# Kernel optimization log

Hardware: AMD Instinct MI355X
Metric: run time of the kernel (lower is better)

## Reference

```python
import jax, jax.numpy as jnp
import numpy as np

D, H, DK, L, F, V = 512, 16, 32, 16, 1024, 32768
C1, C2, CORE, LG, MD, B = 512, 256, 256, 64, 64, 16
T_IN = C1 + C2 + CORE      # 1024
T_TF = CORE + LG + MD      # 384


def _ln(x, g, b, eps=1e-5):
    mu = x.mean(-1, keepdims=True)
    var = ((x - mu) ** 2).mean(-1, keepdims=True)
    return (x - mu) * jax.lax.rsqrt(var + eps) * g + b


def _heads(x):  # [B,T,D] -> [B,H,T,DK]
    b, t, _ = x.shape
    return x.reshape(b, t, H, DK).transpose(0, 2, 1, 3)


def _summarizer(ids, sem, pos, inw, inb, outw, outb, tok, lng, lnb):
    b, t = ids.shape
    x = sem[ids] + pos[:t][None]                      # [B,T,D]
    wq, wk, wv = jnp.split(inw, 3, axis=0)
    bq, bk, bv = jnp.split(inb, 3, axis=0)
    q = _heads(jnp.broadcast_to(tok, (b, tok.shape[1], D)) @ wq.T + bq)
    k = _heads(x @ wk.T + bk)
    v = _heads(x @ wv.T + bv)
    s = jnp.einsum('bhqd,bhkd->bhqk', q, k) / jnp.sqrt(jnp.float32(DK))
    a = jax.nn.softmax(s, axis=-1)
    o = jnp.einsum('bhqk,bhkd->bhqd', a, v).transpose(0, 2, 1, 3).reshape(b, -1, D)
    return _ln(o @ outw.T + outb, lng, lnb)


def _forward(emb_sem, emb_pos,
             lg_sem, lg_pos, lg_inw, lg_inb, lg_outw, lg_outb, lg_tok, lg_lng, lg_lnb,
             md_sem, md_pos, md_inw, md_inb, md_outw, md_outb, md_tok, md_lng, md_lnb,
             qkv_w, qkv_b, wo_w, wo_b, ln1_g, ln1_b, ln2_g, ln2_b,
             ff1_w, ff1_b, ff2_w, ff2_b, hd_lng, hd_lnb, hd_w, hd_b,
             input_ids, target_ids):
    lg_ids = input_ids[:, -(C1 + C2 + CORE):-(C2 + CORE)]
    md_ids = input_ids[:, -(C2 + CORE):-CORE]
    core_ids = input_ids[:, -CORE:]
    tgt = target_ids[:, -CORE:]

    lg_emb = _summarizer(lg_ids, lg_sem, lg_pos, lg_inw, lg_inb, lg_outw, lg_outb, lg_tok, lg_lng, lg_lnb)
    md_emb = _summarizer(md_ids, md_sem, md_pos, md_inw, md_inb, md_outw, md_outb, md_tok, md_lng, md_lnb)
    x_core = emb_sem[core_ids] + emb_pos[:CORE][None]
    x = jnp.concatenate([lg_emb, md_emb, x_core], axis=1)   # [B, 384, D]

    mask = jnp.tril(jnp.ones((T_TF, T_TF), dtype=bool))

    def step(x, p):
        qw, qb, ow, ob, g1, b1, g2, b2, f1w, f1b, f2w, f2b = p
        h = _ln(x, g1, b1)
        qkv = h @ qw.T + qb
        q, k, v = (_heads(t) for t in jnp.split(qkv, 3, axis=-1))
        s = jnp.einsum('bhqd,bhkd->bhqk', q, k) / jnp.sqrt(jnp.float32(DK))
        s = jnp.where(mask, s, -jnp.inf)
        a = jax.nn.softmax(s, axis=-1)
        o = jnp.einsum('bhqk,bhkd->bhqd', a, v).transpose(0, 2, 1, 3).reshape(x.shape)
        x = x + o @ ow.T + ob
        h2 = _ln(x, g2, b2)
        ff = jax.nn.gelu(h2 @ f1w.T + f1b, approximate=False) @ f2w.T + f2b
        return x + ff, None

    x, _ = jax.lax.scan(step, x, (qkv_w, qkv_b, wo_w, wo_b, ln1_g, ln1_b,
                                  ln2_g, ln2_b, ff1_w, ff1_b, ff2_w, ff2_b))
    logits = (_ln(x, hd_lng, hd_lnb) @ hd_w.T + hd_b)[:, -CORE:, :]
    return logits, tgt


def setup_inputs() -> dict:
    key = jax.random.key(0)
    ks = jax.random.split(key, 24)
    def rn(k, shape, s=0.02):
        return jax.random.normal(k, shape, jnp.float32) * s
    z, o = jnp.zeros, jnp.ones
    return {
        'input_ids': jax.random.randint(ks[0], (B, T_IN), 0, V),
        'target_ids': jax.random.randint(ks[1], (B, T_IN), 0, V),
        'emb_sem': rn(ks[2], (V, D)), 'emb_pos': rn(ks[3], (CORE, D)),
        'lg_sem': rn(ks[4], (V, D)), 'lg_pos': rn(ks[5], (C1, D)),
        'lg_inw': rn(ks[6], (3 * D, D)), 'lg_inb': z(3 * D),
        'lg_outw': rn(ks[7], (D, D)), 'lg_outb': z(D),
        'lg_tok': rn(ks[8], (1, LG, D), 1.0), 'lg_lng': o(D), 'lg_lnb': z(D),
        'md_sem': rn(ks[9], (V, D)), 'md_pos': rn(ks[10], (C2, D)),
        'md_inw': rn(ks[11], (3 * D, D)), 'md_inb': z(3 * D),
        'md_outw': rn(ks[12], (D, D)), 'md_outb': z(D),
        'md_tok': rn(ks[13], (1, MD, D), 1.0), 'md_lng': o(D), 'md_lnb': z(D),
        'qkv_w': rn(ks[14], (L, 3 * D, D)), 'qkv_b': z((L, 3 * D)),
        'wo_w': rn(ks[15], (L, D, D)), 'wo_b': z((L, D)),
        'ln1_g': o((L, D)), 'ln1_b': z((L, D)), 'ln2_g': o((L, D)), 'ln2_b': z((L, D)),
        'ff1_w': rn(ks[16], (L, F, D)), 'ff1_b': z((L, F)),
        'ff2_w': rn(ks[17], (L, D, F)), 'ff2_b': z((L, D)),
        'hd_lng': o(D), 'hd_lnb': z(D), 'hd_w': rn(ks[18], (V, D)), 'hd_b': z(V),
    }


def reference(input_ids, target_ids, emb_sem, emb_pos,
              lg_sem, lg_pos, lg_inw, lg_inb, lg_outw, lg_outb, lg_tok, lg_lng, lg_lnb,
              md_sem, md_pos, md_inw, md_inb, md_outw, md_outb, md_tok, md_lng, md_lnb,
              qkv_w, qkv_b, wo_w, wo_b, ln1_g, ln1_b, ln2_g, ln2_b,
              ff1_w, ff1_b, ff2_w, ff2_b, hd_lng, hd_lnb, hd_w, hd_b):
    return _forward(emb_sem, emb_pos,
                    lg_sem, lg_pos, lg_inw, lg_inb, lg_outw, lg_outb, lg_tok, lg_lng, lg_lnb,
                    md_sem, md_pos, md_inw, md_inb, md_outw, md_outb, md_tok, md_lng, md_lnb,
                    qkv_w, qkv_b, wo_w, wo_b, ln1_g, ln1_b, ln2_g, ln2_b,
                    ff1_w, ff1_b, ff2_w, ff2_b, hd_lng, hd_lnb, hd_w, hd_b,
                    input_ids, target_ids)
```

## Files before the change

kernel.cpp:

```cpp
#include <hip/hip_runtime.h>
#include <hip/hip_bf16.h>
#include <math.h>

#define D 512
#define NHEAD 16
#define DK 32
#define NLAYER 16
#define FF 1024
#define VOC 32768
#define TTF 384
#define NCORE 256
#define NB 16

typedef __attribute__((ext_vector_type(8))) short bfrag;
typedef __attribute__((ext_vector_type(4))) float f32x4;

typedef __attribute__((address_space(3))) void lds_void;
typedef const __attribute__((address_space(1))) void gbl_void;
__device__ __forceinline__ void gload16(const void* g, void* l) {
    __builtin_amdgcn_global_load_lds((gbl_void*)g, (lds_void*)l, 16, 0, 0);
}

__device__ __forceinline__ float gelu_f(float v) {
    return 0.5f * v * (1.0f + erff(v * 0.70710678118654752f));
}

__global__ __launch_bounds__(256) void cvt_k(const float* __restrict__ in,
                                             __hip_bfloat16* __restrict__ out, int n)
{
    int i = (blockIdx.x * 256 + threadIdx.x) * 8;
    if (i >= n) return;
    float4 a = *reinterpret_cast<const float4*>(in + i);
    float4 b = *reinterpret_cast<const float4*>(in + i + 4);
    __align__(16) __hip_bfloat16 t[8];
    t[0] = __float2bfloat16(a.x); t[1] = __float2bfloat16(a.y);
    t[2] = __float2bfloat16(a.z); t[3] = __float2bfloat16(a.w);
    t[4] = __float2bfloat16(b.x); t[5] = __float2bfloat16(b.y);
    t[6] = __float2bfloat16(b.z); t[7] = __float2bfloat16(b.w);
    *reinterpret_cast<uint4*>(out + i) = *reinterpret_cast<const uint4*>(t);
}

__global__ __launch_bounds__(256) void cvtpad_k(const float* __restrict__ in,
                                                __hip_bfloat16* __restrict__ out, int n, int ntot)
{
    int i = (blockIdx.x * 256 + threadIdx.x) * 8;
    if (i >= ntot) return;
    __align__(16) __hip_bfloat16 t[8];
    if (i < n) {
        float4 a = *reinterpret_cast<const float4*>(in + i);
        float4 b = *reinterpret_cast<const float4*>(in + i + 4);
        t[0] = __float2bfloat16(a.x); t[1] = __float2bfloat16(a.y);
        t[2] = __float2bfloat16(a.z); t[3] = __float2bfloat16(a.w);
        t[4] = __float2bfloat16(b.x); t[5] = __float2bfloat16(b.y);
        t[6] = __float2bfloat16(b.z); t[7] = __float2bfloat16(b.w);
    } else {
        #pragma unroll
        for (int e = 0; e < 8; e++) t[e] = __float2bfloat16(0.f);
    }
    *reinterpret_cast<uint4*>(out + i) = *reinterpret_cast<const uint4*>(t);
}

template<int OB>
__global__ __launch_bounds__(128) void embed_k(
    const int* __restrict__ ids, int id_stride, int id_off,
    const float* __restrict__ sem, const float* __restrict__ pos,
    void* __restrict__ out, int out_stride, int out_off)
{
    int t = blockIdx.x, b = blockIdx.y, tid = threadIdx.x;
    int id = ids[b * id_stride + id_off + t];
    const float4* s4 = reinterpret_cast<const float4*>(sem + (size_t)id * D);
    const float4* p4 = reinterpret_cast<const float4*>(pos + (size_t)t * D);
    size_t row = (size_t)(b * out_stride + out_off + t) * D;
    float4 a = s4[tid], p = p4[tid];
    float v0 = a.x + p.x, v1 = a.y + p.y, v2 = a.z + p.z, v3 = a.w + p.w;
    if (OB) {
        __hip_bfloat16* o = (__hip_bfloat16*)out + row + tid * 4;
        o[0] = __float2bfloat16(v0); o[1] = __float2bfloat16(v1);
        o[2] = __float2bfloat16(v2); o[3] = __float2bfloat16(v3);
    } else {
        float4* o4 = reinterpret_cast<float4*>((float*)out + row);
        o4[tid] = make_float4(v0, v1, v2, v3);
    }
}

__global__ __launch_bounds__(256) void mgemm_k(
    const __hip_bfloat16* __restrict__ A, const __hip_bfloat16* __restrict__ W,
    const float* __restrict__ bias, void* __restrict__ C,
    int M, int N, int K, int flags, int order, int RT)
{
    __shared__ __align__(16) __hip_bfloat16 sA[2][8192];
    __shared__ __align__(16) __hip_bfloat16 sB[2][8192];
    int tid = threadIdx.x;
    int w = tid >> 6, lane = tid & 63;
    int wr = w >> 1, wc = w & 1;

    int nbx = gridDim.x, nby = gridDim.y;
    int nwg = nbx * nby;
    int bid0 = blockIdx.y * nbx + blockIdx.x;
    int bid = bid0;
    if (nwg >= 8) {
        int q = nwg >> 3, r = nwg & 7;
        int xcd = bid0 & 7, lb = bid0 >> 3;
        bid = (xcd < r ? xcd * (q + 1) : r * (q + 1) + (xcd - r) * q) + lb;
    }
    int bx, byg;
    if (order == 1) { bx = bid / nby; byg = bid - bx * nby; }
    else            { byg = bid / nbx; bx = bid - byg * nbx; }
    int col0 = bx * 128;

    int srow = lane >> 3;
    int scg  = (lane & 7) ^ srow;
    int cr = lane >> 4;
    int cc = lane & 15;

    const __hip_bfloat16* gB[4];
    #pragma unroll
    for (int r = 0; r < 4; r++) {
        int blk = r * 4 + w;
        gB[r] = W + (size_t)(col0 + blk * 8 + srow) * K + scg * 8;
    }

    for (int t = 0; t < RT; t++) {
        int row0 = (byg * RT + t) * 128;

        const __hip_bfloat16* gA[4];
        #pragma unroll
        for (int r = 0; r < 4; r++) {
            int blk = r * 4 + w;
            gA[r] = A + (size_t)(row0 + blk * 8 + srow) * K + scg * 8;
        }

        f32x4 acc[4][4];
        #pragma unroll
        for (int m = 0; m < 4; m++)
            #pragma unroll
            for (int n = 0; n < 4; n++) acc[m][n] = (f32x4){0.f, 0.f, 0.f, 0.f};

        auto stage = [&](int buf, int k0) {
            #pragma unroll
            for (int r = 0; r < 4; r++) {
                int blk = r * 4 + w;
                gload16(gA[r] + k0, &sA[buf][blk * 512]);
                gload16(gB[r] + k0, &sB[buf][blk * 512]);
            }
        };

        stage(0, 0);
        for (int k0 = 0; k0 < K; k0 += 64) {
            int p = (k0 >> 6) & 1;
            bool more = (k0 + 64 < K);
            if (more) {
                stage(p ^ 1, k0 + 64);
                asm volatile("s_waitcnt vmcnt(8)" ::: "memory");
            } else {
                asm volatile("s_waitcnt vmcnt(0)" ::: "memory");
            }
            __builtin_amdgcn_sched_barrier(0);
            __builtin_amdgcn_s_barrier();
            __builtin_amdgcn_sched_barrier(0);

            #pragma unroll
            for (int ks = 0; ks < 2; ks++) {
                bfrag af[4], bf[4];
                #pragma unroll
                for (int m = 0; m < 4; m++) {
                    int blk = wr * 8 + m * 2 + (cc >> 3);
                    int slot = (ks * 4 + cr) ^ (cc & 7);
                    af[m] = *reinterpret_cast<const bfrag*>(&sA[p][blk * 512 + (cc & 7) * 64 + slot * 8]);
                }
                #pragma unroll
                for (int n = 0; n < 4; n++) {
                    int blk = wc * 8 + n * 2 + (cc >> 3);
                    int slot = (ks * 4 + cr) ^ (cc & 7);
                    bf[n] = *reinterpret_cast<const bfrag*>(&sB[p][blk * 512 + (cc & 7) * 64 + slot * 8]);
                }
                #pragma unroll
                for (int m = 0; m < 4; m++)
                    #pragma unroll
                    for (int n = 0; n < 4; n++)
                        acc[m][n] = __builtin_amdgcn_mfma_f32_16x16x32_bf16(af[m], bf[n], acc[m][n], 0, 0, 0);
            }
            __builtin_amdgcn_sched_barrier(0);
            __builtin_amdgcn_s_barrier();
            __builtin_amdgcn_sched_barrier(0);
        }

        #pragma unroll
        for (int m = 0; m < 4; m++) {
            int rg = row0 + wr * 64 + m * 16 + cr * 4;
            #pragma unroll
            for (int n = 0; n < 4; n++) {
                int cg = col0 + wc * 64 + n * 16 + cc;
                float bs = bias[cg];
                #pragma unroll
                for (int j = 0; j < 4; j++) {
                    float v = acc[m][n][j] + bs;
                    size_t off = (size_t)(rg + j) * N + cg;
                    if (flags == 1)      ((float*)C)[off] += v;
                    else if (flags == 2) ((__hip_bfloat16*)C)[off] = __float2bfloat16(gelu_f(v));
                    else if (flags == 3) ((__hip_bfloat16*)C)[off] = __float2bfloat16(v);
                    else                 ((float*)C)[off] = v;
                }
            }
        }
        if (t + 1 < RT) {
            __builtin_amdgcn_s_barrier();
        }
    }
}

template<int OB>
__global__ __launch_bounds__(256) void ln_k(
    const float* __restrict__ in, void* __restrict__ out,
    const float* __restrict__ g, const float* __restrict__ bt,
    int rpb, int in_stride, int in_off, int out_stride, int out_off)
{
    int r = blockIdx.x * 4 + (threadIdx.x >> 6);
    int b = r / rpb, t = r % rpb;
    const float* xr = in + (size_t)(b * in_stride + in_off + t) * D;
    size_t orow = (size_t)(b * out_stride + out_off + t) * D;
    int lane = threadIdx.x & 63;
    float v[8];
    float s = 0.f;
    #pragma unroll
    for (int i = 0; i < 8; i++) { v[i] = xr[lane + i * 64]; s += v[i]; }
    #pragma unroll
    for (int off = 32; off; off >>= 1) s += __shfl_xor(s, off);
    float mu = s * (1.f / 512.f);
    float vs = 0.f;
    #pragma unroll
    for (int i = 0; i < 8; i++) { float d = v[i] - mu; vs += d * d; }
    #pragma unroll
    for (int off = 32; off; off >>= 1) vs += __shfl_xor(vs, off);
    float rstd = rsqrtf(vs * (1.f / 512.f) + 1e-5f);
    #pragma unroll
    for (int i = 0; i < 8; i++) {
        int c = lane + i * 64;
        float y = (v[i] - mu) * rstd * g[c] + bt[c];
        if (OB) ((__hip_bfloat16*)out)[orow + c] = __float2bfloat16(y);
        else    ((float*)out)[orow + c] = y;
    }
}

__global__ __launch_bounds__(512) void fattn_k(
    const __hip_bfloat16* __restrict__ qkv, __hip_bfloat16* __restrict__ o)
{
    __shared__ __align__(16) __hip_bfloat16 Kl[24 * 512];
    __shared__ __align__(16) __hip_bfloat16 Vl[24 * 512];
    __shared__ __align__(16) __hip_bfloat16 Pl[8 * 512];
    int h = blockIdx.x, b = blockIdx.y;
    int tid = threadIdx.x, w = tid >> 6, l = tid & 63;
    const size_t base = (size_t)b * TTF * 1536 + h * DK;

    for (int it = 0; it < 3; it++) {
        int item = it * 512 + tid;
        int key = item >> 2, dg = item & 3;
        uint4 k4 = *reinterpret_cast<const uint4*>(qkv + base + (size_t)key * 1536 + 512 + dg * 8);
        *reinterpret_cast<uint4*>(&Kl[((key >> 4) * 64 + dg * 16 + (key & 15)) * 8]) = k4;
        uint4 v4 = *reinterpret_cast<const uint4*>(qkv + base + (size_t)key * 1536 + 1024 + dg * 8);
        const ushort* ve = reinterpret_cast<const ushort*>(&v4);
        #pragma unroll
        for (int e = 0; e < 8; e++) {
            int dk = dg * 8 + e;
            int f = (((key & 31) >> 3) << 4) | (dk & 15);
            int idx = (((key >> 5) << 1) + (dk >> 4)) * 512 + f * 8 + (key & 7);
            reinterpret_cast<ushort*>(Vl)[idx] = ve[e];
        }
    }
    __syncthreads();

    const float sc = 0.17677669529663687f;
    __hip_bfloat16* pw = Pl + w * 512;

    for (int iq = 0; iq < 3; iq++) {
        int qt = (iq == 0) ? w : (iq == 1 ? 15 - w : 16 + w);
        int q0 = qt * 16;
        bfrag qf = *reinterpret_cast<const bfrag*>(qkv + base + (size_t)(q0 + (l & 15)) * 1536 + (l >> 4) * 8);
        f32x4 oa0 = (f32x4){0.f, 0.f, 0.f, 0.f};
        f32x4 oa1 = (f32x4){0.f, 0.f, 0.f, 0.f};
        float mrun[4], lrun[4];
        #pragma unroll
        for (int jj = 0; jj < 4; jj++) { mrun[jj] = -3.0e38f; lrun[jj] = 0.f; }
        int ksmax = (q0 + 15) >> 5;

        for (int ks = 0; ks <= ksmax; ks++) {
            bfrag kf0 = *reinterpret_cast<const bfrag*>(&Kl[(ks * 2 + 0) * 512 + l * 8]);
            bfrag kf1 = *reinterpret_cast<const bfrag*>(&Kl[(ks * 2 + 1) * 512 + l * 8]);
            f32x4 z = (f32x4){0.f, 0.f, 0.f, 0.f};
            f32x4 s0 = __builtin_amdgcn_mfma_f32_16x16x32_bf16(qf, kf0, z, 0, 0, 0);
            f32x4 s1 = __builtin_amdgcn_mfma_f32_16x16x32_bf16(qf, kf1, z, 0, 0, 0);
            if (ks == ksmax) {
                #pragma unroll
                for (int jj = 0; jj < 4; jj++) {
                    int q = q0 + ((l >> 4) << 2) + jj;
                    if (ks * 32 + (l & 15) > q)      s0[jj] = -3.0e38f;
                    if (ks * 32 + 16 + (l & 15) > q) s1[jj] = -3.0e38f;
                }
            }
            float p0[4], p1[4], ps[4];
            #pragma unroll
            for (int jj = 0; jj < 4; jj++) {
                float sm = fmaxf(s0[jj], s1[jj]);
                #pragma unroll
                for (int off = 1; off <= 8; off <<= 1) sm = fmaxf(sm, __shfl_xor(sm, off));
                float mnew = fmaxf(mrun[jj], sm);
                float f = __expf((mrun[jj] - mnew) * sc);
                mrun[jj] = mnew;
                lrun[jj] *= f;
                oa0[jj] *= f; oa1[jj] *= f;
                p0[jj] = __expf((s0[jj] - mnew) * sc);
                p1[jj] = __expf((s1[jj] - mnew) * sc);
                ps[jj] = p0[jj] + p1[jj];
            }
            #pragma unroll
            for (int jj = 0; jj < 4; jj++) {
                float t = ps[jj];
                #pragma unroll
                for (int off = 1; off <= 8; off <<= 1) t += __shfl_xor(t, off);
                lrun[jj] += t;
            }
            #pragma unroll
            for (int jj = 0; jj < 4; jj++) {
                int ql = ((l >> 4) << 2) + jj;
                int kl0 = l & 15, kl1 = 16 + (l & 15);
                pw[((kl0 >> 3) * 16 + ql) * 8 + (kl0 & 7)] = __float2bfloat16(p0[jj]);
                pw[((kl1 >> 3) * 16 + ql) * 8 + (kl1 & 7)] = __float2bfloat16(p1[jj]);
            }
            bfrag pf  = *reinterpret_cast<const bfrag*>(&pw[l * 8]);
            bfrag vf0 = *reinterpret_cast<const bfrag*>(&Vl[(ks * 2 + 0) * 512 + l * 8]);
            bfrag vf1 = *reinterpret_cast<const bfrag*>(&Vl[(ks * 2 + 1) * 512 + l * 8]);
            oa0 = __builtin_amdgcn_mfma_f32_16x16x32_bf16(pf, vf0, oa0, 0, 0, 0);
            oa1 = __builtin_amdgcn_mfma_f32_16x16x32_bf16(pf, vf1, oa1, 0, 0, 0);
        }
        #pragma unroll
        for (int jj = 0; jj < 4; jj++) {
            float inv = 1.0f / lrun[jj];
            int q = q0 + ((l >> 4) << 2) + jj;
            size_t orow = ((size_t)b * TTF + q) * D + h * DK;
            o[orow + (l & 15)]      = __float2bfloat16(oa0[jj] * inv);
            o[orow + 16 + (l & 15)] = __float2bfloat16(oa1[jj] * inv);
        }
    }
}

template<int TLEN>
__global__ __launch_bounds__(256) void sattn_k(
    const __hip_bfloat16* __restrict__ q, const __hip_bfloat16* __restrict__ kv,
    __hip_bfloat16* __restrict__ o)
{
    __shared__ __align__(16) __hip_bfloat16 Kl[(TLEN / 16) * 512];
    __shared__ __align__(16) __hip_bfloat16 Vl[(TLEN / 16) * 512];
    __shared__ __align__(16) __hip_bfloat16 Pl[4 * 512];
    int h = blockIdx.x, b = blockIdx.y;
    int tid = threadIdx.x, w = tid >> 6, l = tid & 63;

    for (int it = 0; it < TLEN / 64; it++) {
        int item = it * 256 + tid;
        int key = item >> 2, dg = item & 3;
        const __hip_bfloat16* kr = kv + (size_t)(b * TLEN + key) * 1024 + h * DK + dg * 8;
        uint4 k4 = *reinterpret_cast<const uint4*>(kr);
        *reinterpret_cast<uint4*>(&Kl[((key >> 4) * 64 + dg * 16 + (key & 15)) * 8]) = k4;
        uint4 v4 = *reinterpret_cast<const uint4*>(kr + 512);
        const ushort* ve = reinterpret_cast<const ushort*>(&v4);
        #pragma unroll
        for (int e = 0; e < 8; e++) {
            int dk = dg * 8 + e;
            int f = (((key & 31) >> 3) << 4) | (dk & 15);
            int idx = (((key >> 5) << 1) + (dk >> 4)) * 512 + f * 8 + (key & 7);
            reinterpret_cast<ushort*>(Vl)[idx] = ve[e];
        }
    }
    __syncthreads();

    const float sc = 0.17677669529663687f;
    __hip_bfloat16* pw = Pl + w * 512;
    int q0 = w * 16;
    bfrag qf = *reinterpret_cast<const bfrag*>(q + (size_t)(q0 + (l & 15)) * D + h * DK + (l >> 4) * 8);
    f32x4 oa0 = (f32x4){0.f, 0.f, 0.f, 0.f};
    f32x4 oa1 = (f32x4){0.f, 0.f, 0.f, 0.f};
    float mrun[4], lrun[4];
    #pragma unroll
    for (int jj = 0; jj < 4; jj++) { mrun[jj] = -3.0e38f; lrun[jj] = 0.f; }

    for (int ks = 0; ks < TLEN / 32; ks++) {
        bfrag kf0 = *reinterpret_cast<const bfrag*>(&Kl[(ks * 2 + 0) * 512 + l * 8]);
        bfrag kf1 = *reinterpret_cast<const bfrag*>(&Kl[(ks * 2 + 1) * 512 + l * 8]);
        f32x4 z = (f32x4){0.f, 0.f, 0.f, 0.f};
        f32x4 s0 = __builtin_amdgcn_mfma_f32_16x16x32_bf16(qf, kf0, z, 0, 0, 0);
        f32x4 s1 = __builtin_amdgcn_mfma_f32_16x16x32_bf16(qf, kf1, z, 0, 0, 0);
        float p0[4], p1[4], ps[4];
        #pragma unroll
        for (int jj = 0; jj < 4; jj++) {
            float sm = fmaxf(s0[jj], s1[jj]);
            #pragma unroll
            for (int off = 1; off <= 8; off <<= 1) sm = fmaxf(sm, __shfl_xor(sm, off));
            float mnew = fmaxf(mrun[jj], sm);
            float f = __expf((mrun[jj] - mnew) * sc);
            mrun[jj] = mnew;
            lrun[jj] *= f;
            oa0[jj] *= f; oa1[jj] *= f;
            p0[jj] = __expf((s0[jj] - mnew) * sc);
            p1[jj] = __expf((s1[jj] - mnew) * sc);
            ps[jj] = p0[jj] + p1[jj];
        }
        #pragma unroll
        for (int jj = 0; jj < 4; jj++) {
            float t = ps[jj];
            #pragma unroll
            for (int off = 1; off <= 8; off <<= 1) t += __shfl_xor(t, off);
            lrun[jj] += t;
        }
        #pragma unroll
        for (int jj = 0; jj < 4; jj++) {
            int ql = ((l >> 4) << 2) + jj;
            int kl0 = l & 15, kl1 = 16 + (l & 15);
            pw[((kl0 >> 3) * 16 + ql) * 8 + (kl0 & 7)] = __float2bfloat16(p0[jj]);
            pw[((kl1 >> 3) * 16 + ql) * 8 + (kl1 & 7)] = __float2bfloat16(p1[jj]);
        }
        bfrag pf  = *reinterpret_cast<const bfrag*>(&pw[l * 8]);
        bfrag vf0 = *reinterpret_cast<const bfrag*>(&Vl[(ks * 2 + 0) * 512 + l * 8]);
        bfrag vf1 = *reinterpret_cast<const bfrag*>(&Vl[(ks * 2 + 1) * 512 + l * 8]);
        oa0 = __builtin_amdgcn_mfma_f32_16x16x32_bf16(pf, vf0, oa0, 0, 0, 0);
        oa1 = __builtin_amdgcn_mfma_f32_16x16x32_bf16(pf, vf1, oa1, 0, 0, 0);
    }
    #pragma unroll
    for (int jj = 0; jj < 4; jj++) {
        float inv = 1.0f / lrun[jj];
        int qi = q0 + ((l >> 4) << 2) + jj;
        size_t orow = ((size_t)b * 64 + qi) * D + h * DK;
        o[orow + (l & 15)]      = __float2bfloat16(oa0[jj] * inv);
        o[orow + 16 + (l & 15)] = __float2bfloat16(oa1[jj] * inv);
    }
}

__global__ __launch_bounds__(256) void tgt_k(const int* __restrict__ tids, float* __restrict__ out)
{
    int i = blockIdx.x * 256 + threadIdx.x;
    int b = i >> 8, c = i & 255;
    out[i] = (float)tids[b * 1024 + 768 + c];
}

extern "C" void kernel_launch(void* const* d_in, const int* in_sizes, int n_in,
                              void* d_out, int out_size, void* d_ws, size_t ws_size,
                              hipStream_t stream) {
    (void)in_sizes; (void)n_in; (void)out_size; (void)ws_size;
    const int*   input_ids  = (const int*)  d_in[0];
    const int*   target_ids = (const int*)  d_in[1];
    const float* emb_sem    = (const float*)d_in[2];
    const float* emb_pos    = (const float*)d_in[3];
    const float* lg_sem     = (const float*)d_in[4];
    const float* lg_pos     = (const float*)d_in[5];
    const float* lg_inw     = (const float*)d_in[6];
    const float* lg_inb     = (const float*)d_in[7];
    const float* lg_outw    = (const float*)d_in[8];
    const float* lg_outb    = (const float*)d_in[9];
    const float* lg_tok     = (const float*)d_in[10];
    const float* lg_lng     = (const float*)d_in[11];
    const float* lg_lnb     = (const float*)d_in[12];
    const float* md_sem     = (const float*)d_in[13];
    const float* md_pos     = (const float*)d_in[14];
    const float* md_inw     = (const float*)d_in[15];
    const float* md_inb     = (const float*)d_in[16];
    const float* md_outw    = (const float*)d_in[17];
    const float* md_outb    = (const float*)d_in[18];
    const float* md_tok     = (const float*)d_in[19];
    const float* md_lng     = (const float*)d_in[20];
    const float* md_lnb     = (const float*)d_in[21];
    const float* qkv_w      = (const float*)d_in[22];
    const float* qkv_b      = (const float*)d_in[23];
    const float* wo_w       = (const float*)d_in[24];
    const float* wo_b       = (const float*)d_in[25];
    const float* ln1_g      = (const float*)d_in[26];
    const float* ln1_b      = (const float*)d_in[27];
    const float* ln2_g      = (const float*)d_in[28];
    const float* ln2_b      = (const float*)d_in[29];
    const float* ff1_w      = (const float*)d_in[30];
    const float* ff1_b      = (const float*)d_in[31];
    const float* ff2_w      = (const float*)d_in[32];
    const float* ff2_b      = (const float*)d_in[33];
    const float* hd_lng     = (const float*)d_in[34];
    const float* hd_lnb     = (const float*)d_in[35];
    const float* hd_w       = (const float*)d_in[36];
    const float* hd_b       = (const float*)d_in[37];

    float* x    = (float*)d_ws;
    float* qkvb = x    + 3145728;
    float* so2  = qkvb + 9437184;
    float* q_s  = so2  + 524288;
    __hip_bfloat16* qkv_bf = (__hip_bfloat16*)qkvb;
    __hip_bfloat16* h_bf   = (__hip_bfloat16*)(q_s + 32768);
    __hip_bfloat16* a_bf   = h_bf   + 3145728;
    __hip_bfloat16* sumo_bf= a_bf   + 6291456;
    __hip_bfloat16* w_qkv  = sumo_bf+ 524288;
    __hip_bfloat16* w_wo   = w_qkv  + 12582912;
    __hip_bfloat16* w_ff1  = w_wo   + 4194304;
    __hip_bfloat16* w_ff2  = w_ff1  + 8388608;
    __hip_bfloat16* w_hd   = w_ff2  + 8388608;
    __hip_bfloat16* w_lgin = w_hd   + 16777216;
    __hip_bfloat16* w_mdin = w_lgin + 786432;
    __hip_bfloat16* w_lgout= w_mdin + 786432;
    __hip_bfloat16* w_mdout= w_lgout+ 262144;
    __hip_bfloat16* tok_lg = w_mdout+ 262144;
    __hip_bfloat16* tok_md = tok_lg + 65536;
    __hip_bfloat16* q_bf   = tok_md + 65536;

    cvt_k<<<12582912 / 2048, 256, 0, stream>>>(qkv_w, w_qkv, 12582912);
    cvt_k<<< 4194304 / 2048, 256, 0, stream>>>(wo_w,  w_wo,   4194304);
    cvt_k<<< 8388608 / 2048, 256, 0, stream>>>(ff1_w, w_ff1,  8388608);
    cvt_k<<< 8388608 / 2048, 256, 0, stream>>>(ff2_w, w_ff2,  8388608);
    cvt_k<<<16777216 / 2048, 256, 0, stream>>>(hd_w,  w_hd,  16777216);
    cvt_k<<<  786432 / 2048, 256, 0, stream>>>(lg_inw, w_lgin, 786432);
    cvt_k<<<  786432 / 2048, 256, 0, stream>>>(md_inw, w_mdin, 786432);
    cvt_k<<<  262144 / 2048, 256, 0, stream>>>(lg_outw, w_lgout, 262144);
    cvt_k<<<  262144 / 2048, 256, 0, stream>>>(md_outw, w_mdout, 262144);
    cvtpad_k<<<32, 256, 0, stream>>>(lg_tok, tok_lg, 32768, 65536);
    cvtpad_k<<<32, 256, 0, stream>>>(md_tok, tok_md, 32768, 65536);

    embed_k<1><<<dim3(512, NB), 128, 0, stream>>>(input_ids, 1024, 0, lg_sem, lg_pos, a_bf, 512, 0);
    mgemm_k<<<dim3(8, 64), 256, 0, stream>>>(a_bf, w_lgin + 512 * 512, lg_inb + 512, qkv_bf, 8192, 1024, 512, 3, 0, 1);
    mgemm_k<<<dim3(4, 1), 256, 0, stream>>>(tok_lg, w_lgin, lg_inb, q_bf, 128, 512, 512, 3, 0, 1);
    sattn_k<512><<<dim3(NHEAD, NB), 256, 0, stream>>>(q_bf, qkv_bf, sumo_bf);
    mgemm_k<<<dim3(4, 8), 256, 0, stream>>>(sumo_bf, w_lgout, lg_outb, so2, 1024, 512, 512, 0, 0, 1);
    ln_k<0><<<256, 256, 0, stream>>>(so2, x, lg_lng, lg_lnb, 64, 64, 0, TTF, 0);

    embed_k<1><<<dim3(256, NB), 128, 0, stream>>>(input_ids, 1024, 512, md_sem, md_pos, a_bf, 256, 0);
    mgemm_k<<<dim3(8, 32), 256, 0, stream>>>(a_bf, w_mdin + 512 * 512, md_inb + 512, qkv_bf, 4096, 1024, 512, 3, 0, 1);
    mgemm_k<<<dim3(4, 1), 256, 0, stream>>>(tok_md, w_mdin, md_inb, q_bf, 128, 512, 512, 3, 0, 1);
    sattn_k<256><<<dim3(NHEAD, NB), 256, 0, stream>>>(q_bf, qkv_bf, sumo_bf);
    mgemm_k<<<dim3(4, 8), 256, 0, stream>>>(sumo_bf, w_mdout, md_outb, so2, 1024, 512, 512, 0, 0, 1);
    ln_k<0><<<256, 256, 0, stream>>>(so2, x, md_lng, md_lnb, 64, 64, 0, TTF, 64);

    embed_k<0><<<dim3(256, NB), 128, 0, stream>>>(input_ids, 1024, 768, emb_sem, emb_pos, x, TTF, 128);

    for (int l = 0; l < NLAYER; l++) {
        ln_k<1><<<1536, 256, 0, stream>>>(x, h_bf, ln1_g + l * D, ln1_b + l * D, TTF, TTF, 0, TTF, 0);
        mgemm_k<<<dim3(12, 48), 256, 0, stream>>>(h_bf, w_qkv + (size_t)l * 1536 * 512, qkv_b + l * 1536, qkv_bf, 6144, 1536, 512, 3, 0, 1);
        fattn_k<<<dim3(NHEAD, NB), 512, 0, stream>>>(qkv_bf, a_bf);
        mgemm_k<<<dim3(4, 48), 256, 0, stream>>>(a_bf, w_wo + (size_t)l * 512 * 512, wo_b + l * D, x, 6144, 512, 512, 1, 0, 1);
        ln_k<1><<<1536, 256, 0, stream>>>(x, h_bf, ln2_g + l * D, ln2_b + l * D, TTF, TTF, 0, TTF, 0);
        mgemm_k<<<dim3(8, 48), 256, 0, stream>>>(h_bf, w_ff1 + (size_t)l * 1024 * 512, ff1_b + l * FF, a_bf, 6144, 1024, 512, 2, 0, 1);
        mgemm_k<<<dim3(4, 48), 256, 0, stream>>>(a_bf, w_ff2 + (size_t)l * 512 * 1024, ff2_b + l * D, x, 6144, 512, 1024, 1, 0, 1);
    }

    ln_k<1><<<1024, 256, 0, stream>>>(x, h_bf, hd_lng, hd_lnb, NCORE, TTF, 128, NCORE, 0);
    float* logits = (float*)d_out;
    mgemm_k<<<dim3(256, 8), 256, 0, stream>>>(h_bf, w_hd, hd_b, logits, 4096, VOC, 512, 0, 1, 4);
    tgt_k<<<16, 256, 0, stream>>>(target_ids, logits + (size_t)NB * NCORE * VOC);
}
```

Baseline: 3.150 ms.

## Keep residual stream in bf16 and fuse residual add with next LayerNorm

The residual stream x moves from fp32 to bf16. The Wo and FF2 GEMMs now write bf16 deltas instead of doing fp32 read-modify-write accumulation. A new res_ln_k kernel adds each delta into x and computes the next LayerNorm in the same pass, replacing the separate LN launches. The LN kernels are vectorized to 16-byte loads and stores. This cuts global memory traffic in the epilogues and LN passes, but rounds the residual to bf16 every layer, which risks accuracy drift across 16 layers.

```diff
diff --git a/kernel.cpp b/kernel.cpp
--- a/kernel.cpp
+++ b/kernel.cpp
@@ -25,19 +25,28 @@
     return 0.5f * v * (1.0f + erff(v * 0.70710678118654752f));
 }
 
+__device__ __forceinline__ void bf8_to_f32(uint4 u, float* v) {
+    const __hip_bfloat16* t = reinterpret_cast<const __hip_bfloat16*>(&u);
+    #pragma unroll
+    for (int e = 0; e < 8; e++) v[e] = __bfloat162float(t[e]);
+}
+__device__ __forceinline__ uint4 f32_to_bf8(const float* v) {
+    uint4 u; __hip_bfloat16* t = reinterpret_cast<__hip_bfloat16*>(&u);
+    #pragma unroll
+    for (int e = 0; e < 8; e++) t[e] = __float2bfloat16(v[e]);
+    return u;
+}
+
 __global__ __launch_bounds__(256) void cvt_k(const float* __restrict__ in,
                                              __hip_bfloat16* __restrict__ out, int n)
 {
     int i = (blockIdx.x * 256 + threadIdx.x) * 8;
     if (i >= n) return;
+    float v[8];
     float4 a = *reinterpret_cast<const float4*>(in + i);
     float4 b = *reinterpret_cast<const float4*>(in + i + 4);
-    __align__(16) __hip_bfloat16 t[8];
-    t[0] = __float2bfloat16(a.x); t[1] = __float2bfloat16(a.y);
-    t[2] = __float2bfloat16(a.z); t[3] = __float2bfloat16(a.w);
-    t[4] = __float2bfloat16(b.x); t[5] = __float2bfloat16(b.y);
-    t[6] = __float2bfloat16(b.z); t[7] = __float2bfloat16(b.w);
-    *reinterpret_cast<uint4*>(out + i) = *reinterpret_cast<const uint4*>(t);
+    v[0]=a.x; v[1]=a.y; v[2]=a.z; v[3]=a.w; v[4]=b.x; v[5]=b.y; v[6]=b.z; v[7]=b.w;
+    *reinterpret_cast<uint4*>(out + i) = f32_to_bf8(v);
 }
 
 __global__ __launch_bounds__(256) void cvtpad_k(const float* __restrict__ in,
@@ -45,26 +54,19 @@
 {
     int i = (blockIdx.x * 256 + threadIdx.x) * 8;
     if (i >= ntot) return;
-    __align__(16) __hip_bfloat16 t[8];
+    float v[8] = {0.f,0.f,0.f,0.f,0.f,0.f,0.f,0.f};
     if (i < n) {
         float4 a = *reinterpret_cast<const float4*>(in + i);
         float4 b = *reinterpret_cast<const float4*>(in + i + 4);
-        t[0] = __float2bfloat16(a.x); t[1] = __float2bfloat16(a.y);
-        t[2] = __float2bfloat16(a.z); t[3] = __float2bfloat16(a.w);
-        t[4] = __float2bfloat16(b.x); t[5] = __float2bfloat16(b.y);
-        t[6] = __float2bfloat16(b.z); t[7] = __float2bfloat16(b.w);
-    } else {
-        #pragma unroll
-        for (int e = 0; e < 8; e++) t[e] = __float2bfloat16(0.f);
-    }
-    *reinterpret_cast<uint4*>(out + i) = *reinterpret_cast<const uint4*>(t);
-}
-
-template<int OB>
+        v[0]=a.x; v[1]=a.y; v[2]=a.z; v[3]=a.w; v[4]=b.x; v[5]=b.y; v[6]=b.z; v[7]=b.w;
+    }
+    *reinterpret_cast<uint4*>(out + i) = f32_to_bf8(v);
+}
+
 __global__ __launch_bounds__(128) void embed_k(
     const int* __restrict__ ids, int id_stride, int id_off,
     const float* __restrict__ sem, const float* __restrict__ pos,
-    void* __restrict__ out, int out_stride, int out_off)
+    __hip_bfloat16* __restrict__ out, int out_stride, int out_off)
 {
     int t = blockIdx.x, b = blockIdx.y, tid = threadIdx.x;
     int id = ids[b * id_stride + id_off + t];
@@ -72,15 +74,9 @@
     const float4* p4 = reinterpret_cast<const float4*>(pos + (size_t)t * D);
     size_t row = (size_t)(b * out_stride + out_off + t) * D;
     float4 a = s4[tid], p = p4[tid];
-    float v0 = a.x + p.x, v1 = a.y + p.y, v2 = a.z + p.z, v3 = a.w + p.w;
-    if (OB) {
-        __hip_bfloat16* o = (__hip_bfloat16*)out + row + tid * 4;
-        o[0] = __float2bfloat16(v0); o[1] = __float2bfloat16(v1);
-        o[2] = __float2bfloat16(v2); o[3] = __float2bfloat16(v3);
-    } else {
-        float4* o4 = reinterpret_cast<float4*>((float*)out + row);
-        o4[tid] = make_float4(v0, v1, v2, v3);
-    }
+    __hip_bfloat16* o = out + row + tid * 4;
+    o[0] = __float2bfloat16(a.x + p.x); o[1] = __float2bfloat16(a.y + p.y);
+    o[2] = __float2bfloat16(a.z + p.z); o[3] = __float2bfloat16(a.w + p.w);
 }
 
 __global__ __launch_bounds__(256) void mgemm_k(
@@ -196,8 +192,7 @@
                 for (int j = 0; j < 4; j++) {
                     float v = acc[m][n][j] + bs;
                     size_t off = (size_t)(rg + j) * N + cg;
-                    if (flags == 1)      ((float*)C)[off] += v;
-                    else if (flags == 2) ((__hip_bfloat16*)C)[off] = __float2bfloat16(gelu_f(v));
+                    if (flags == 2)      ((__hip_bfloat16*)C)[off] = __float2bfloat16(gelu_f(v));
                     else if (flags == 3) ((__hip_bfloat16*)C)[off] = __float2bfloat16(v);
                     else                 ((float*)C)[off] = v;
                 }
@@ -209,36 +204,80 @@
     }
 }
 
-template<int OB>
+template<int IB, int OB>
 __global__ __launch_bounds__(256) void ln_k(
-    const float* __restrict__ in, void* __restrict__ out,
+    const void* __restrict__ in, void* __restrict__ out,
     const float* __restrict__ g, const float* __restrict__ bt,
     int rpb, int in_stride, int in_off, int out_stride, int out_off)
 {
     int r = blockIdx.x * 4 + (threadIdx.x >> 6);
     int b = r / rpb, t = r % rpb;
-    const float* xr = in + (size_t)(b * in_stride + in_off + t) * D;
+    size_t irow = (size_t)(b * in_stride + in_off + t) * D;
     size_t orow = (size_t)(b * out_stride + out_off + t) * D;
-    int lane = threadIdx.x & 63;
+    int c0 = (threadIdx.x & 63) * 8;
     float v[8];
+    if (IB) {
+        bf8_to_f32(*reinterpret_cast<const uint4*>((const __hip_bfloat16*)in + irow + c0), v);
+    } else {
+        float4 a = *reinterpret_cast<const float4*>((const float*)in + irow + c0);
+        float4 bq = *reinterpret_cast<const float4*>((const float*)in + irow + c0 + 4);
+        v[0]=a.x; v[1]=a.y; v[2]=a.z; v[3]=a.w; v[4]=bq.x; v[5]=bq.y; v[6]=bq.z; v[7]=bq.w;
+    }
     float s = 0.f;
     #pragma unroll
-    for (int i = 0; i < 8; i++) { v[i] = xr[lane + i * 64]; s += v[i]; }
+    for (int e = 0; e < 8; e++) s += v[e];
     #pragma unroll
     for (int off = 32; off; off >>= 1) s += __shfl_xor(s, off);
     float mu = s * (1.f / 512.f);
     float vs = 0.f;
     #pragma unroll
-    for (int i = 0; i < 8; i++) { float d = v[i] - mu; vs += d * d; }
+    for (int e = 0; e < 8; e++) { float d = v[e] - mu; vs += d * d; }
     #pragma unroll
     for (int off = 32; off; off >>= 1) vs += __shfl_xor(vs, off);
     float rstd = rsqrtf(vs * (1.f / 512.f) + 1e-5f);
-    #pragma unroll
-    for (int i = 0; i < 8; i++) {
-        int c = lane + i * 64;
-        float y = (v[i] - mu) * rstd * g[c] + bt[c];
-        if (OB) ((__hip_bfloat16*)out)[orow + c] = __float2bfloat16(y);
-        else    ((float*)out)[orow + c] = y;
+    float y[8];
+    #pragma unroll
+    for (int e = 0; e < 8; e++) y[e] = (v[e] - mu) * rstd * g[c0 + e] + bt[c0 + e];
+    if (OB) {
+        *reinterpret_cast<uint4*>((__hip_bfloat16*)out + orow + c0) = f32_to_bf8(y);
+    } else {
+        *reinterpret_cast<float4*>((float*)out + orow + c0)     = make_float4(y[0], y[1], y[2], y[3]);
+        *reinterpret_cast<float4*>((float*)out + orow + c0 + 4) = make_float4(y[4], y[5], y[6], y[7]);
+    }
+}
+
+template<int WRITE_H>
+__global__ __launch_bounds__(256) void res_ln_k(
+    const __hip_bfloat16* __restrict__ delta, __hip_bfloat16* __restrict__ x,
+    const float* __restrict__ g, const float* __restrict__ bt,
+    __hip_bfloat16* __restrict__ h)
+{
+    int r = blockIdx.x * 4 + (threadIdx.x >> 6);
+    int c0 = (threadIdx.x & 63) * 8;
+    size_t row = (size_t)r * D + c0;
+    float v[8], dv[8];
+    bf8_to_f32(*reinterpret_cast<const uint4*>(x + row), v);
+    bf8_to_f32(*reinterpret_cast<const uint4*>(delta + row), dv);
+    #pragma unroll
+    for (int e = 0; e < 8; e++) v[e] += dv[e];
+    *reinterpret_cast<uint4*>(x + row) = f32_to_bf8(v);
+    if (WRITE_H) {
+        float s = 0.f;
+        #pragma unroll
+        for (int e = 0; e < 8; e++) s += v[e];
+        #pragma unroll
+        for (int off = 32; off; off >>= 1) s += __shfl_xor(s, off);
+        float mu = s * (1.f / 512.f);
+        float vs = 0.f;
+        #pragma unroll
+        for (int e = 0; e < 8; e++) { float d = v[e] - mu; vs += d * d; }
+        #pragma unroll
+        for (int off = 32; off; off >>= 1) vs += __shfl_xor(vs, off);
+        float rstd = rsqrtf(vs * (1.f / 512.f) + 1e-5f);
+        float y[8];
+        #pragma unroll
+        for (int e = 0; e < 8; e++) y[e] = (v[e] - mu) * rstd * g[c0 + e] + bt[c0 + e];
+        *reinterpret_cast<uint4*>(h + row) = f32_to_bf8(y);
     }
 }
 
@@ -483,14 +522,12 @@
     const float* hd_w       = (const float*)d_in[36];
     const float* hd_b       = (const float*)d_in[37];
 
-    float* x    = (float*)d_ws;
-    float* qkvb = x    + 3145728;
-    float* so2  = qkvb + 9437184;
-    float* q_s  = so2  + 524288;
-    __hip_bfloat16* qkv_bf = (__hip_bfloat16*)qkvb;
-    __hip_bfloat16* h_bf   = (__hip_bfloat16*)(q_s + 32768);
-    __hip_bfloat16* a_bf   = h_bf   + 3145728;
-    __hip_bfloat16* sumo_bf= a_bf   + 6291456;
+    __hip_bfloat16* x_bf   = (__hip_bfloat16*)d_ws;
+    __hip_bfloat16* h_bf   = x_bf   + 3145728;
+    __hip_bfloat16* d_bf   = h_bf   + 3145728;
+    __hip_bfloat16* a_bf   = d_bf   + 3145728;
+    __hip_bfloat16* qkv_bf = a_bf   + 6291456;
+    __hip_bfloat16* sumo_bf= qkv_bf + 9437184;
     __hip_bfloat16* w_qkv  = sumo_bf+ 524288;
     __hip_bfloat16* w_wo   = w_qkv  + 12582912;
     __hip_bfloat16* w_ff1  = w_wo   + 4194304;
@@ -503,6 +540,7 @@
     __hip_bfloat16* tok_lg = w_mdout+ 262144;
     __hip_bfloat16* tok_md = tok_lg + 65536;
     __hip_bfloat16* q_bf   = tok_md + 65536;
+    float* so2 = (float*)(q_bf + 65536);
 
     cvt_k<<<12582912 / 2048, 256, 0, stream>>>(qkv_w, w_qkv, 12582912);
     cvt_k<<< 4194304 / 2048, 256, 0, stream>>>(wo_w,  w_wo,   4194304);
@@ -516,33 +554,38 @@
     cvtpad_k<<<32, 256, 0, stream>>>(lg_tok, tok_lg, 32768, 65536);
     cvtpad_k<<<32, 256, 0, stream>>>(md_tok, tok_md, 32768, 65536);
 
-    embed_k<1><<<dim3(512, NB), 128, 0, stream>>>(input_ids, 1024, 0, lg_sem, lg_pos, a_bf, 512, 0);
+    embed_k<<<dim3(512, NB), 128, 0, stream>>>(input_ids, 1024, 0, lg_sem, lg_pos, a_bf, 512, 0);
     mgemm_k<<<dim3(8, 64), 256, 0, stream>>>(a_bf, w_lgin + 512 * 512, lg_inb + 512, qkv_bf, 8192, 1024, 512, 3, 0, 1);
     mgemm_k<<<dim3(4, 1), 256, 0, stream>>>(tok_lg, w_lgin, lg_inb, q_bf, 128, 512, 512, 3, 0, 1);
     sattn_k<512><<<dim3(NHEAD, NB), 256, 0, stream>>>(q_bf, qkv_bf, sumo_bf);
     mgemm_k<<<dim3(4, 8), 256, 0, stream>>>(sumo_bf, w_lgout, lg_outb, so2, 1024, 512, 512, 0, 0, 1);
-    ln_k<0><<<256, 256, 0, stream>>>(so2, x, lg_lng, lg_lnb, 64, 64, 0, TTF, 0);
-
-    embed_k<1><<<dim3(256, NB), 128, 0, stream>>>(input_ids, 1024, 512, md_sem, md_pos, a_bf, 256, 0);
+    ln_k<0, 1><<<256, 256, 0, stream>>>(so2, x_bf, lg_lng, lg_lnb, 64, 64, 0, TTF, 0);
+
+    embed_k<<<dim3(256, NB), 128, 0, stream>>>(input_ids, 1024, 512, md_sem, md_pos, a_bf, 256, 0);
     mgemm_k<<<dim3(8, 32), 256, 0, stream>>>(a_bf, w_mdin + 512 * 512, md_inb + 512, qkv_bf, 4096, 1024, 512, 3, 0, 1);
     mgemm_k<<<dim3(4, 1), 256, 0, stream>>>(tok_md, w_mdin, md_inb, q_bf, 128, 512, 512, 3, 0, 1);
     sattn_k<256><<<dim3(NHEAD, NB), 256, 0, stream>>>(q_bf, qkv_bf, sumo_bf);
     mgemm_k<<<dim3(4, 8), 256, 0, stream>>>(sumo_bf, w_mdout, md_outb, so2, 1024, 512, 512, 0, 0, 1);
-    ln_k<0><<<256, 256, 0, stream>>>(so2, x, md_lng, md_lnb, 64, 64, 0, TTF, 64);
-
-    embed_k<0><<<dim3(256, NB), 128, 0, stream>>>(input_ids, 1024, 768, emb_sem, emb_pos, x, TTF, 128);
-
+    ln_k<0, 1><<<256, 256, 0, stream>>>(so2, x_bf, md_lng, md_lnb, 64, 64, 0, TTF, 64);
+
+    embed_k<<<dim3(256, NB), 128, 0, stream>>>(input_ids, 1024, 768, emb_sem, emb_pos, x_bf, TTF, 128);
+
+    ln_k<1, 1><<<1536, 256, 0, stream>>>(x_bf, h_bf, ln1_g, ln1_b, TTF, TTF, 0, TTF, 0);
     for (int l = 0; l < NLAYER; l++) {
-        ln_k<1><<<1536, 256, 0, stream>>>(x, h_bf, ln1_g + l * D, ln1_b + l * D, TTF, TTF, 0, TTF, 0);
         mgemm_k<<<dim3(12, 48), 256, 0, stream>>>(h_bf, w_qkv + (size_t)l * 1536 * 512, qkv_b + l * 1536, qkv_bf, 6144, 1536, 512, 3, 0, 1);
         fattn_k<<<dim3(NHEAD, NB), 512, 0, stream>>>(qkv_bf, a_bf);
-        mgemm_k<<<dim3(4, 48), 256, 0, stream>>>(a_bf, w_wo + (size_t)l * 512 * 512, wo_b + l * D, x, 6144, 512, 512, 1, 0, 1);
-        ln_k<1><<<1536, 256, 0, stream>>>(x, h_bf, ln2_g + l * D, ln2_b + l * D, TTF, TTF, 0, TTF, 0);
+        mgemm_k<<<dim3(4, 48), 256, 0, stream>>>(a_bf, w_wo + (size_t)l * 512 * 512, wo_b + l * D, d_bf, 6144, 512, 512, 3, 0, 1);
+        res_ln_k<1><<<1536, 256, 0, stream>>>(d_bf, x_bf, ln2_g + l * D, ln2_b + l * D, h_bf);
         mgemm_k<<<dim3(8, 48), 256, 0, stream>>>(h_bf, w_ff1 + (size_t)l * 1024 * 512, ff1_b + l * FF, a_bf, 6144, 1024, 512, 2, 0, 1);
-        mgemm_k<<<dim3(4, 48), 256, 0, stream>>>(a_bf, w_ff2 + (size_t)l * 512 * 1024, ff2_b + l * D, x, 6144, 512, 1024, 1, 0, 1);
-    }
-
-    ln_k<1><<<1024, 256, 0, stream>>>(x, h_bf, hd_lng, hd_lnb, NCORE, TTF, 128, NCORE, 0);
+        mgemm_k<<<dim3(4, 48), 256, 0, stream>>>(a_bf, w_ff2 + (size_t)l * 512 * 1024, ff2_b + l * D, d_bf, 6144, 512, 1024, 3, 0, 1);
+        if (l < NLAYER - 1) {
+            res_ln_k<1><<<1536, 256, 0, stream>>>(d_bf, x_bf, ln1_g + (size_t)(l + 1) * D, ln1_b + (size_t)(l + 1) * D, h_bf);
+        } else {
+            res_ln_k<0><<<1536, 256, 0, stream>>>(d_bf, x_bf, hd_lng, hd_lnb, h_bf);
+        }
+    }
+
+    ln_k<1, 1><<<1024, 256, 0, stream>>>(x_bf, h_bf, hd_lng, hd_lnb, NCORE, TTF, 128, NCORE, 0);
     float* logits = (float*)d_out;
     mgemm_k<<<dim3(256, 8), 256, 0, stream>>>(h_bf, w_hd, hd_b, logits, 4096, VOC, 512, 0, 1, 4);
     tgt_k<<<16, 256, 0, stream>>>(target_ids, logits + (size_t)NB * NCORE * VOC);
```

New measurement: 2.735 ms. 13.2% less time.
